# Optimization experiments

Measured on AMD Instinct MI355X. Metric: run time of the kernel, lower is better.

## Reference

```python
import jax, jax.numpy as jnp
import numpy as np

B, N, C = 2, 10000, 128
NH, NP = 4, 20          # n_heads, n_points (n_levels = 1)
DH = C // NH            # head dim = 32
HW = 100                # spatial shape (100, 100), N = HW*HW


def setup_inputs() -> dict:
    key = jax.random.key(0)
    ks = jax.random.split(key, 12)
    s = 0.05  # small param scale so softmax/linears stay well-conditioned
    return {
        "query": jax.random.normal(ks[0], (B, N, C), jnp.float32),
        "query_pos": jax.random.normal(ks[1], (B, N, C), jnp.float32),
        "W_val": jax.random.normal(ks[2], (C, C), jnp.float32) * s,
        "b_val": jax.random.normal(ks[3], (C,), jnp.float32) * s,
        "W_off": jax.random.normal(ks[4], (NH * NP * 2, C), jnp.float32) * s,
        "b_off": jax.random.normal(ks[5], (NH * NP * 2,), jnp.float32) * s,
        "W_attn": jax.random.normal(ks[6], (NH * NP, C), jnp.float32) * s,
        "b_attn": jax.random.normal(ks[7], (NH * NP,), jnp.float32) * s,
        "W_out1": jax.random.normal(ks[8], (C, C), jnp.float32) * s,
        "b_out1": jax.random.normal(ks[9], (C,), jnp.float32) * s,
        "W_out2": jax.random.normal(ks[10], (C, C), jnp.float32) * s,
        "b_out2": jax.random.normal(ks[11], (C,), jnp.float32) * s,
    }


def _msdeform_forward(query, query_pos, W_val, b_val, W_off, b_off,
                      W_attn, b_attn, W_out1, b_out1, W_out2, b_out2):
    residual = query
    q = query + query_pos  # pos added; value branch also uses q (query.clone())

    # reference points: meshgrid of (z, x) normalized to (0,1), shape (N, 2)
    lin = (jnp.arange(HW, dtype=jnp.float32) + 0.5) / HW
    ref_z, ref_x = jnp.meshgrid(lin, lin, indexing="ij")
    ref = jnp.stack([ref_z.reshape(-1), ref_x.reshape(-1)], axis=-1)  # (N,2)

    # projections
    value = (q @ W_val.T + b_val).reshape(B, N, NH, DH).transpose(0, 2, 1, 3)  # (B,NH,N,DH)
    off = (q @ W_off.T + b_off).reshape(B, N, NH, NP, 2)
    attn = jax.nn.softmax((q @ W_attn.T + b_attn).reshape(B, N, NH, NP), axis=-1)

    # sampling locations in normalized coords; offset normalizer = (W, H) = (100, 100)
    loc = ref[None, :, None, None, :] + off / HW  # (B,N,NH,NP,2)

    # grid_sample bilinear, align_corners=False, zeros padding:
    # pixel coord = loc * size - 0.5
    x = (loc[..., 0] * HW - 0.5).transpose(0, 2, 1, 3)  # (B,NH,N,NP)
    y = (loc[..., 1] * HW - 0.5).transpose(0, 2, 1, 3)
    aw = attn.transpose(0, 2, 1, 3)                     # (B,NH,N,NP)

    x0f = jnp.floor(x); y0f = jnp.floor(y)
    wx1 = x - x0f; wy1 = y - y0f
    wx0 = 1.0 - wx1; wy0 = 1.0 - wy1
    ix0 = x0f.astype(jnp.int32); iy0 = y0f.astype(jnp.int32)
    ix1 = ix0 + 1; iy1 = iy0 + 1

    def gather(ix, iy):
        valid = ((ix >= 0) & (ix < HW) & (iy >= 0) & (iy < HW)).astype(value.dtype)
        idx = jnp.clip(iy, 0, HW - 1) * HW + jnp.clip(ix, 0, HW - 1)  # (B,NH,N,NP)
        g = jnp.take_along_axis(value, idx.reshape(B, NH, N * NP, 1), axis=2)
        return g.reshape(B, NH, N, NP, DH) * valid[..., None]

    sampled = ((wx0 * wy0)[..., None] * gather(ix0, iy0)
               + (wx1 * wy0)[..., None] * gather(ix1, iy0)
               + (wx0 * wy1)[..., None] * gather(ix0, iy1)
               + (wx1 * wy1)[..., None] * gather(ix1, iy1))  # (B,NH,N,NP,DH)

    out = (sampled * aw[..., None]).sum(axis=3)             # (B,NH,N,DH)
    out = out.transpose(0, 2, 1, 3).reshape(B, N, C)
    out = out @ W_out1.T + b_out1   # MSDeformAttn.output_proj
    out = out @ W_out2.T + b_out2   # wrapper output_proj
    return out + residual           # dropout is identity in eval


def reference(query, query_pos, W_val, b_val, W_off, b_off,
              W_attn, b_attn, W_out1, b_out1, W_out2, b_out2):
    return _msdeform_forward(query, query_pos, W_val, b_val, W_off, b_off,
                             W_attn, b_attn, W_out1, b_out1, W_out2, b_out2)
```

## Files before the change

### kernel.cpp

```cpp
#include <hip/hip_runtime.h>
#include <hip/hip_bf16.h>
#include <math.h>

#define NTOK 10000
#define BATCH 2
#define CDIM 128
#define NHEAD 4
#define NPNT 20
#define DHEAD 32
#define HWDIM 100
#define MROWS (BATCH * NTOK)
#define OPAD 384
#define PHALO 4
#define TTILE 4
#define SPD 12
#define NPT 25
#define CELLPAD 40

typedef __attribute__((ext_vector_type(8))) short short8v;
typedef __attribute__((ext_vector_type(4))) short short4v;
typedef __attribute__((ext_vector_type(4))) float f32x4;

__device__ __forceinline__ float asf(unsigned u) {
  union { unsigned u; float f; } c; c.u = u; return c.f;
}

__device__ __forceinline__ void acc_cell(const __hip_bfloat16* p, float w,
                                         f32x4& a0, f32x4& a1) {
  int4 u = *(const int4*)p;
  f32x4 g0, g1;
  g0.x = asf(((unsigned)u.x) << 16); g0.y = asf(((unsigned)u.x) & 0xFFFF0000u);
  g0.z = asf(((unsigned)u.y) << 16); g0.w = asf(((unsigned)u.y) & 0xFFFF0000u);
  g1.x = asf(((unsigned)u.z) << 16); g1.y = asf(((unsigned)u.z) & 0xFFFF0000u);
  g1.z = asf(((unsigned)u.w) << 16); g1.w = asf(((unsigned)u.w) & 0xFFFF0000u);
  a0 += g0 * w;
  a1 += g1 * w;
}

__global__ __launch_bounds__(128) void prep_kernel(
    const float* __restrict__ W_val, const float* __restrict__ b_val,
    const float* __restrict__ W_off, const float* __restrict__ b_off,
    const float* __restrict__ W_attn, const float* __restrict__ b_attn,
    const float* __restrict__ W1, const float* __restrict__ b1,
    const float* __restrict__ W2, const float* __restrict__ b2,
    __hip_bfloat16* __restrict__ Wcat, float* __restrict__ bcat,
    __hip_bfloat16* __restrict__ Wc_bf, float* __restrict__ bc) {
  __shared__ float w2row[128];
  __shared__ float red[128];
  const int blk = blockIdx.x, c = threadIdx.x;
  if (blk < OPAD) {
    float v = 0.f, bv = 0.f;
    if (blk < 128) {
      v = W_val[blk * 128 + c]; bv = b_val[blk];
    } else {
      int h = (blk - 128) >> 6, k = (blk - 128) & 63;
      if (k < 40) { v = W_off[(h * 40 + k) * 128 + c]; bv = b_off[h * 40 + k]; }
      else if (k < 60) { v = W_attn[(h * 20 + k - 40) * 128 + c]; bv = b_attn[h * 20 + k - 40]; }
    }
    Wcat[(size_t)blk * 128 + c] = __float2bfloat16(v);
    if (c == 0) bcat[blk] = bv;
  } else {
    const int o = blk - OPAD;
    w2row[c] = W2[o * 128 + c];
    __syncthreads();
    float acc = 0.f;
    for (int k = 0; k < 128; ++k) acc += w2row[k] * W1[k * 128 + c];
    Wc_bf[(size_t)o * 128 + c] = __float2bfloat16(acc);
    red[c] = w2row[c] * b1[c];
    __syncthreads();
    for (int s = 64; s > 0; s >>= 1) {
      if (c < s) red[c] += red[c + s];
      __syncthreads();
    }
    if (c == 0) bc[o] = b2[o] + red[0];
  }
}

__global__ __launch_bounds__(256) void proj1_kernel(
    const float* __restrict__ query, const float* __restrict__ qpos,
    const __hip_bfloat16* __restrict__ Wcat, const float* __restrict__ bcat,
    __hip_bfloat16* __restrict__ value, __hip_bfloat16* __restrict__ offb,
    float* __restrict__ attnb) {
  __shared__ __hip_bfloat16 qa[64][128];
  __shared__ __hip_bfloat16 wb[64][128];
  const int t = threadIdx.x;
  const int r0 = blockIdx.x * 64;

#pragma unroll
  for (int i = 0; i < 4; ++i) {
    int lin = t + 256 * i;
    int r = lin >> 4, g = lin & 15;
    int c = g << 3;
    float4 v0 = make_float4(0.f, 0.f, 0.f, 0.f);
    float4 v1 = make_float4(0.f, 0.f, 0.f, 0.f);
    if (r0 + r < MROWS) {
      const float* p = query + (size_t)(r0 + r) * CDIM + c;
      v0 = *(const float4*)p;
      v1 = *(const float4*)(p + 4);
      const float* p2 = qpos + (size_t)(r0 + r) * CDIM + c;
      float4 u0 = *(const float4*)p2;
      float4 u1 = *(const float4*)(p2 + 4);
      v0.x += u0.x; v0.y += u0.y; v0.z += u0.z; v0.w += u0.w;
      v1.x += u1.x; v1.y += u1.y; v1.z += u1.z; v1.w += u1.w;
    }
    __hip_bfloat16* dst = &qa[r][(g ^ (r & 7)) << 3];
    dst[0] = __float2bfloat16(v0.x); dst[1] = __float2bfloat16(v0.y);
    dst[2] = __float2bfloat16(v0.z); dst[3] = __float2bfloat16(v0.w);
    dst[4] = __float2bfloat16(v1.x); dst[5] = __float2bfloat16(v1.y);
    dst[6] = __float2bfloat16(v1.z); dst[7] = __float2bfloat16(v1.w);
  }
  __syncthreads();

  const int wid = t >> 6;
  const int lane = t & 63;
  const int wr = (wid >> 1) * 32;
  const int wc = (wid & 1) * 32;
  const int lrow = lane & 15;
  const int lk = lane >> 4;

  short8v afr[4][2];
  {
    int ra0 = wr + lrow, ra1 = wr + 16 + lrow;
#pragma unroll
    for (int kk = 0; kk < 4; ++kk) {
      int gb = kk * 4 + lk;
      afr[kk][0] = *(const short8v*)&qa[ra0][(gb ^ (ra0 & 7)) << 3];
      afr[kk][1] = *(const short8v*)&qa[ra1][(gb ^ (ra1 & 7)) << 3];
    }
  }

  for (int ti = 0; ti < 3; ++ti) {
    const int ot = blockIdx.y * 192 + ti * 64;
    __syncthreads();
#pragma unroll
    for (int i = 0; i < 4; ++i) {
      int lin = t + 256 * i;
      int r = lin >> 4, g = lin & 15;
      short8v w = *(const short8v*)(Wcat + (size_t)(ot + r) * 128 + (g << 3));
      *(short8v*)&wb[r][(g ^ (r & 7)) << 3] = w;
    }
    __syncthreads();

    f32x4 acc[2][2];
#pragma unroll
    for (int mi = 0; mi < 2; ++mi)
#pragma unroll
      for (int ni = 0; ni < 2; ++ni) acc[mi][ni] = (f32x4)(0.f);

#pragma unroll
    for (int kk = 0; kk < 4; ++kk) {
      const int gb = kk * 4 + lk;
      int rb0 = wc + lrow, rb1 = wc + 16 + lrow;
      short8v b0 = *(const short8v*)&wb[rb0][(gb ^ (rb0 & 7)) << 3];
      short8v b1 = *(const short8v*)&wb[rb1][(gb ^ (rb1 & 7)) << 3];
      acc[0][0] = __builtin_amdgcn_mfma_f32_16x16x32_bf16(afr[kk][0], b0, acc[0][0], 0, 0, 0);
      acc[0][1] = __builtin_amdgcn_mfma_f32_16x16x32_bf16(afr[kk][0], b1, acc[0][1], 0, 0, 0);
      acc[1][0] = __builtin_amdgcn_mfma_f32_16x16x32_bf16(afr[kk][1], b0, acc[1][0], 0, 0, 0);
      acc[1][1] = __builtin_amdgcn_mfma_f32_16x16x32_bf16(afr[kk][1], b1, acc[1][1], 0, 0, 0);
    }

#pragma unroll
    for (int mi = 0; mi < 2; ++mi) {
#pragma unroll
      for (int ni = 0; ni < 2; ++ni) {
#pragma unroll
        for (int reg = 0; reg < 4; ++reg) {
          int r = r0 + wr + mi * 16 + (lane >> 4) * 4 + reg;
          int o = ot + wc + ni * 16 + (lane & 15);
          if (r >= MROWS) continue;
          float v = acc[mi][ni][reg] + bcat[o];
          int b = r >= NTOK ? 1 : 0;
          int n = r - b * NTOK;
          if (o < 128) {
            int h = o >> 5, rem = o & 31;
            value[(((size_t)b * NHEAD + h) * NTOK + n) * 32 + rem] =
                __float2bfloat16(v);
          } else {
            int h = (o - 128) >> 6, k = (o - 128) & 63;
            size_t base = ((size_t)(b * NHEAD + h) * NTOK + n);
            if (k < 40) {
              offb[base * 40 + k] = __float2bfloat16(v);
            } else if (k < 60) {
              attnb[base * 20 + (k - 40)] = v;
            }
          }
        }
      }
    }
  }
}

__global__ __launch_bounds__(256) void proj2_kernel(
    const __hip_bfloat16* __restrict__ outat,
    const __hip_bfloat16* __restrict__ Wc_bf, const float* __restrict__ bc,
    const float* __restrict__ resid, float* __restrict__ out) {
  __shared__ __hip_bfloat16 qa[64][128];
  __shared__ __hip_bfloat16 wb[64][128];
  const int t = threadIdx.x;
  const int r0 = blockIdx.x * 64;
  const int ot = blockIdx.y * 64;

#pragma unroll
  for (int i = 0; i < 4; ++i) {
    int lin = t + 256 * i;
    int r = lin >> 4, g = lin & 15;
    short8v v = (short8v)(short)0;
    if (r0 + r < MROWS)
      v = *(const short8v*)(outat + (size_t)(r0 + r) * CDIM + (g << 3));
    *(short8v*)&qa[r][(g ^ (r & 7)) << 3] = v;
  }
#pragma unroll
  for (int i = 0; i < 4; ++i) {
    int lin = t + 256 * i;
    int r = lin >> 4, g = lin & 15;
    short8v w = *(const short8v*)(Wc_bf + (size_t)(ot + r) * 128 + (g << 3));
    *(short8v*)&wb[r][(g ^ (r & 7)) << 3] = w;
  }
  __syncthreads();

  const int wid = t >> 6;
  const int lane = t & 63;
  const int wr = (wid >> 1) * 32;
  const int wc = (wid & 1) * 32;
  const int lrow = lane & 15;
  const int lk = lane >> 4;

  f32x4 acc[2][2];
#pragma unroll
  for (int mi = 0; mi < 2; ++mi)
#pragma unroll
    for (int ni = 0; ni < 2; ++ni) acc[mi][ni] = (f32x4)(0.f);

#pragma unroll
  for (int kk = 0; kk < 4; ++kk) {
    const int gb = kk * 4 + lk;
    int ra0 = wr + lrow, ra1 = wr + 16 + lrow;
    int rb0 = wc + lrow, rb1 = wc + 16 + lrow;
    short8v a0 = *(const short8v*)&qa[ra0][(gb ^ (ra0 & 7)) << 3];
    short8v a1 = *(const short8v*)&qa[ra1][(gb ^ (ra1 & 7)) << 3];
    short8v b0 = *(const short8v*)&wb[rb0][(gb ^ (rb0 & 7)) << 3];
    short8v b1 = *(const short8v*)&wb[rb1][(gb ^ (rb1 & 7)) << 3];
    acc[0][0] = __builtin_amdgcn_mfma_f32_16x16x32_bf16(a0, b0, acc[0][0], 0, 0, 0);
    acc[0][1] = __builtin_amdgcn_mfma_f32_16x16x32_bf16(a0, b1, acc[0][1], 0, 0, 0);
    acc[1][0] = __builtin_amdgcn_mfma_f32_16x16x32_bf16(a1, b0, acc[1][0], 0, 0, 0);
    acc[1][1] = __builtin_amdgcn_mfma_f32_16x16x32_bf16(a1, b1, acc[1][1], 0, 0, 0);
  }

#pragma unroll
  for (int mi = 0; mi < 2; ++mi) {
#pragma unroll
    for (int ni = 0; ni < 2; ++ni) {
#pragma unroll
      for (int reg = 0; reg < 4; ++reg) {
        int r = r0 + wr + mi * 16 + (lane >> 4) * 4 + reg;
        int o = ot + wc + ni * 16 + (lane & 15);
        if (r >= MROWS) continue;
        out[(size_t)r * CDIM + o] =
            acc[mi][ni][reg] + bc[o] + resid[(size_t)r * CDIM + o];
      }
    }
  }
}

__global__ __launch_bounds__(256) void sample_kernel(
    const __hip_bfloat16* __restrict__ value,
    const __hip_bfloat16* __restrict__ off, const float* __restrict__ attn,
    __hip_bfloat16* __restrict__ outat) {
  const int s = blockIdx.x & 7;
  const int pidx = blockIdx.x >> 3;
  const int PI = pidx % NPT, PJ = pidx / NPT;
  const int I0 = PI * TTILE, J0 = PJ * TTILE;
  const int b = s >> 2, h = s & 3;

  __shared__ __hip_bfloat16 patch[SPD * SPD][CELLPAD];
  const __hip_bfloat16* vglob = value + (size_t)s * NTOK * DHEAD;

  const int t = threadIdx.x;
  const int lane16 = t & 15;
  const int dg = lane16 & 3;
  const int pg = lane16 >> 2;
  const int tok = t >> 4;
  const int li = tok & 3, lj = tok >> 2;
  const int i = I0 + li, j = J0 + lj;
  const int n = i * HWDIM + j;

  unsigned ofu[5];
  float atf[5];
  {
    const unsigned* ob =
        (const unsigned*)(off + ((size_t)s * NTOK + n) * 40) + pg * 5;
    const float* ab = attn + ((size_t)s * NTOK + n) * 20 + pg * 5;
#pragma unroll
    for (int k = 0; k < 5; ++k) { ofu[k] = ob[k]; atf[k] = ab[k]; }
  }

#pragma unroll
  for (int it = 0; it < 3; ++it) {
    int lin = t + 256 * it;
    if (lin < SPD * SPD * 4) {
      int cell = lin >> 2, part = lin & 3;
      int py = cell / SPD, px = cell - py * SPD;
      int gy = J0 - PHALO + py;
      int gx = I0 - PHALO + px;
      short8v v = (short8v)(short)0;
      if (gy >= 0 && gy < HWDIM && gx >= 0 && gx < HWDIM)
        v = *(const short8v*)(vglob + ((size_t)(gy * HWDIM + gx)) * DHEAD +
                              part * 8);
      *(short8v*)&patch[cell][part * 8] = v;
    }
  }
  __syncthreads();

  float ssum = 0.f;
#pragma unroll
  for (int k = 0; k < 5; ++k) {
    atf[k] = __expf(atf[k]);
    ssum += atf[k];
  }

  const float fi = (float)i, fj = (float)j;
  f32x4 a0 = (f32x4)(0.f), a1 = (f32x4)(0.f);
  f32x4 e0 = (f32x4)(0.f), e1 = (f32x4)(0.f);
#pragma unroll
  for (int k = 0; k < 5; ++k) {
    const unsigned up = ofu[k];
    float x = fi + asf(up << 16);
    float y = fj + asf(up & 0xFFFF0000u);
    float aw = atf[k];
    float x0f = floorf(x), y0f = floorf(y);
    int ix0 = (int)x0f, iy0 = (int)y0f;
    float wx1 = x - x0f, wy1 = y - y0f;
    float wx0 = 1.f - wx1, wy0 = 1.f - wy1;
    float wya = aw * wy0, wyb = aw * wy1;
    float w00 = wya * wx0, w01 = wya * wx1;
    float w10 = wyb * wx0, w11 = wyb * wx1;
    int ly = iy0 - (J0 - PHALO);
    int lx = ix0 - (I0 - PHALO);
    if ((unsigned)ly <= SPD - 2 && (unsigned)lx <= SPD - 2) {
      const __hip_bfloat16* pb = &patch[ly * SPD + lx][dg * 8];
      acc_cell(pb, w00, a0, a1);
      acc_cell(pb + CELLPAD, w01, e0, e1);
      acc_cell(pb + SPD * CELLPAD, w10, a0, a1);
      acc_cell(pb + SPD * CELLPAD + CELLPAD, w11, e0, e1);
    } else {
      float wgt[4] = {w00, w01, w10, w11};
#pragma unroll
      for (int cy = 0; cy < 2; ++cy) {
        int iy = iy0 + cy;
        if (iy < 0 || iy >= HWDIM) continue;
#pragma unroll
        for (int cx = 0; cx < 2; ++cx) {
          int ix = ix0 + cx;
          if (ix < 0 || ix >= HWDIM) continue;
          acc_cell(vglob + ((size_t)(iy * HWDIM + ix)) * DHEAD + dg * 8,
                   wgt[cy * 2 + cx], a0, a1);
        }
      }
    }
  }
  f32x4 r0 = a0 + e0;
  f32x4 r1 = a1 + e1;

#pragma unroll
  for (int m = 4; m <= 8; m <<= 1) {
#pragma unroll
    for (int el = 0; el < 4; ++el) {
      r0[el] += __shfl_xor(r0[el], m);
      r1[el] += __shfl_xor(r1[el], m);
    }
    ssum += __shfl_xor(ssum, m);
  }

  if (pg == 0) {
    const float inv = 1.f / ssum;
    union { short8v v8; __hip_bfloat16 hh[8]; } o;
#pragma unroll
    for (int k = 0; k < 4; ++k) {
      o.hh[k] = __float2bfloat16(r0[k] * inv);
      o.hh[4 + k] = __float2bfloat16(r1[k] * inv);
    }
    *(short8v*)(outat + ((size_t)b * NTOK + n) * CDIM + h * DHEAD + dg * 8) =
        o.v8;
  }
}

extern "C" void kernel_launch(void* const* d_in, const int* in_sizes, int n_in,
                              void* d_out, int out_size, void* d_ws,
                              size_t ws_size, hipStream_t stream) {
  const float* query = (const float*)d_in[0];
  const float* query_pos = (const float*)d_in[1];
  const float* W_val = (const float*)d_in[2];
  const float* b_val = (const float*)d_in[3];
  const float* W_off = (const float*)d_in[4];
  const float* b_off = (const float*)d_in[5];
  const float* W_attn = (const float*)d_in[6];
  const float* b_attn = (const float*)d_in[7];
  const float* W_out1 = (const float*)d_in[8];
  const float* b_out1 = (const float*)d_in[9];
  const float* W_out2 = (const float*)d_in[10];
  const float* b_out2 = (const float*)d_in[11];
  float* out = (float*)d_out;

  char* ws = (char*)d_ws;
  __hip_bfloat16* value = (__hip_bfloat16*)ws;
  ws += (size_t)MROWS * CDIM * 2;
  __hip_bfloat16* offb = (__hip_bfloat16*)ws;
  ws += (size_t)MROWS * 160 * 2;
  float* attnb = (float*)ws;
  ws += (size_t)MROWS * 80 * 4;
  __hip_bfloat16* outat = (__hip_bfloat16*)ws;
  ws += (size_t)MROWS * CDIM * 2;
  float* bcat = (float*)ws; ws += OPAD * 4;
  float* bc = (float*)ws; ws += 128 * 4;
  __hip_bfloat16* Wcat = (__hip_bfloat16*)ws; ws += (size_t)OPAD * 128 * 2;
  __hip_bfloat16* Wc_bf = (__hip_bfloat16*)ws;

  prep_kernel<<<OPAD + 128, 128, 0, stream>>>(
      W_val, b_val, W_off, b_off, W_attn, b_attn, W_out1, b_out1, W_out2,
      b_out2, Wcat, bcat, Wc_bf, bc);

  proj1_kernel<<<dim3(313, 2), 256, 0, stream>>>(query, query_pos, Wcat, bcat,
                                                 value, offb, attnb);

  sample_kernel<<<8 * NPT * NPT, 256, 0, stream>>>(value, offb, attnb, outat);

  proj2_kernel<<<dim3(313, 2), 256, 0, stream>>>(outat, Wc_bf, bc, query, out);
}
```

Baseline: 58.95 us.

## Recast deformable sampling as dense weight-matrix times patch MFMA

The sampling kernel now scatters bilinear×attention weights into a per-token dense weight matrix over a 12x16 shared-memory patch using LDS atomics. It then multiplies that matrix by the transposed value patch with bf16 MFMA instructions. Tiles grow to 4x8 tokens, and out-of-patch samples fall back to per-element atomic accumulation from global memory. This trades the per-thread gather FMA work for matrix-core throughput, at the cost of LDS atomics, a transpose, extra barriers and bf16 rounding of the weights.

```diff
diff --git a/kernel.cpp b/kernel.cpp
--- a/kernel.cpp
+++ b/kernel.cpp
@@ -12,29 +12,20 @@
 #define MROWS (BATCH * NTOK)
 #define OPAD 384
 #define PHALO 4
-#define TTILE 4
-#define SPD 12
-#define NPT 25
-#define CELLPAD 40
+#define TI 4
+#define TJ 8
+#define SPI 12
+#define SPJ 16
+#define NPI 25
+#define NPJ 13
+#define NCELL 192
+#define WBS 200
 
 typedef __attribute__((ext_vector_type(8))) short short8v;
-typedef __attribute__((ext_vector_type(4))) short short4v;
 typedef __attribute__((ext_vector_type(4))) float f32x4;
 
 __device__ __forceinline__ float asf(unsigned u) {
   union { unsigned u; float f; } c; c.u = u; return c.f;
-}
-
-__device__ __forceinline__ void acc_cell(const __hip_bfloat16* p, float w,
-                                         f32x4& a0, f32x4& a1) {
-  int4 u = *(const int4*)p;
-  f32x4 g0, g1;
-  g0.x = asf(((unsigned)u.x) << 16); g0.y = asf(((unsigned)u.x) & 0xFFFF0000u);
-  g0.z = asf(((unsigned)u.y) << 16); g0.w = asf(((unsigned)u.y) & 0xFFFF0000u);
-  g1.x = asf(((unsigned)u.z) << 16); g1.y = asf(((unsigned)u.z) & 0xFFFF0000u);
-  g1.z = asf(((unsigned)u.w) << 16); g1.w = asf(((unsigned)u.w) & 0xFFFF0000u);
-  a0 += g0 * w;
-  a1 += g1 * w;
 }
 
 __global__ __launch_bounds__(128) void prep_kernel(
@@ -268,119 +259,176 @@
     __hip_bfloat16* __restrict__ outat) {
   const int s = blockIdx.x & 7;
   const int pidx = blockIdx.x >> 3;
-  const int PI = pidx % NPT, PJ = pidx / NPT;
-  const int I0 = PI * TTILE, J0 = PJ * TTILE;
+  const int PI = pidx % NPI, PJ = pidx / NPI;
+  const int I0 = PI * TI, J0 = PJ * TJ;
   const int b = s >> 2, h = s & 3;
 
-  __shared__ __hip_bfloat16 patch[SPD * SPD][CELLPAD];
+  __shared__ __align__(16) char smem[24576 + 12800 + 4096];
+  float* Wf = (float*)smem;
+  __hip_bfloat16* Wb = (__hip_bfloat16*)smem;
+  __hip_bfloat16* Vt = (__hip_bfloat16*)(smem + 24576);
+  float* fx = (float*)(smem + 24576 + 12800);
+
   const __hip_bfloat16* vglob = value + (size_t)s * NTOK * DHEAD;
-
   const int t = threadIdx.x;
-  const int lane16 = t & 15;
-  const int dg = lane16 & 3;
-  const int pg = lane16 >> 2;
-  const int tok = t >> 4;
+
+  int4 vl[3];
+#pragma unroll
+  for (int it = 0; it < 3; ++it) {
+    int task = t + 256 * it;
+    int cell = task >> 2, part = task & 3;
+    int py = cell / SPI, px = cell - py * SPI;
+    int gy = J0 - PHALO + py;
+    int gx = I0 - PHALO + px;
+    vl[it] = make_int4(0, 0, 0, 0);
+    if (gy >= 0 && gy < HWDIM && gx >= 0 && gx < HWDIM)
+      vl[it] = *(const int4*)(vglob + ((size_t)(gy * HWDIM + gx)) * DHEAD +
+                              part * 8);
+  }
+
+  const int tok = t >> 3, pg = t & 7;
   const int li = tok & 3, lj = tok >> 2;
   const int i = I0 + li, j = J0 + lj;
-  const int n = i * HWDIM + j;
-
-  unsigned ofu[5];
-  float atf[5];
+  const bool tv = (j < HWDIM);
+  const int n = tv ? (i * HWDIM + j) : 0;
+  unsigned ofu[3];
+  float atf[3];
+  int np = 0;
   {
-    const unsigned* ob =
-        (const unsigned*)(off + ((size_t)s * NTOK + n) * 40) + pg * 5;
-    const float* ab = attn + ((size_t)s * NTOK + n) * 20 + pg * 5;
-#pragma unroll
-    for (int k = 0; k < 5; ++k) { ofu[k] = ob[k]; atf[k] = ab[k]; }
-  }
+    const unsigned* ob = (const unsigned*)(off + ((size_t)s * NTOK + n) * 40);
+    const float* ab = attn + ((size_t)s * NTOK + n) * 20;
+#pragma unroll
+    for (int k = 0; k < 3; ++k) {
+      int p = pg + 8 * k;
+      if (p < NPNT) {
+        ofu[np] = ob[p];
+        atf[np] = ab[p];
+        ++np;
+      }
+    }
+  }
+
+  {
+    float4 z4 = make_float4(0.f, 0.f, 0.f, 0.f);
+    float4* wf4 = (float4*)Wf;
+#pragma unroll
+    for (int it = 0; it < 6; ++it) wf4[t + 256 * it] = z4;
+    ((float4*)fx)[t] = z4;
+  }
+
+  float ssum = 0.f;
+  for (int k = 0; k < np; ++k) { atf[k] = __expf(atf[k]); ssum += atf[k]; }
+  ssum += __shfl_xor(ssum, 1);
+  ssum += __shfl_xor(ssum, 2);
+  ssum += __shfl_xor(ssum, 4);
+  const float inv = tv ? (1.f / ssum) : 0.f;
+
+  __syncthreads();
 
 #pragma unroll
   for (int it = 0; it < 3; ++it) {
-    int lin = t + 256 * it;
-    if (lin < SPD * SPD * 4) {
-      int cell = lin >> 2, part = lin & 3;
-      int py = cell / SPD, px = cell - py * SPD;
-      int gy = J0 - PHALO + py;
-      int gx = I0 - PHALO + px;
-      short8v v = (short8v)(short)0;
-      if (gy >= 0 && gy < HWDIM && gx >= 0 && gx < HWDIM)
-        v = *(const short8v*)(vglob + ((size_t)(gy * HWDIM + gx)) * DHEAD +
-                              part * 8);
-      *(short8v*)&patch[cell][part * 8] = v;
-    }
-  }
-  __syncthreads();
-
-  float ssum = 0.f;
-#pragma unroll
-  for (int k = 0; k < 5; ++k) {
-    atf[k] = __expf(atf[k]);
-    ssum += atf[k];
+    int task = t + 256 * it;
+    int cell = task >> 2, part = task & 3;
+    union { int4 v4; __hip_bfloat16 hh[8]; } u;
+    u.v4 = vl[it];
+    int d0 = part * 8;
+#pragma unroll
+    for (int k = 0; k < 8; ++k) Vt[(d0 + k) * WBS + cell] = u.hh[k];
   }
 
   const float fi = (float)i, fj = (float)j;
-  f32x4 a0 = (f32x4)(0.f), a1 = (f32x4)(0.f);
-  f32x4 e0 = (f32x4)(0.f), e1 = (f32x4)(0.f);
-#pragma unroll
-  for (int k = 0; k < 5; ++k) {
-    const unsigned up = ofu[k];
-    float x = fi + asf(up << 16);
-    float y = fj + asf(up & 0xFFFF0000u);
-    float aw = atf[k];
-    float x0f = floorf(x), y0f = floorf(y);
-    int ix0 = (int)x0f, iy0 = (int)y0f;
-    float wx1 = x - x0f, wy1 = y - y0f;
-    float wx0 = 1.f - wx1, wy0 = 1.f - wy1;
-    float wya = aw * wy0, wyb = aw * wy1;
-    float w00 = wya * wx0, w01 = wya * wx1;
-    float w10 = wyb * wx0, w11 = wyb * wx1;
-    int ly = iy0 - (J0 - PHALO);
-    int lx = ix0 - (I0 - PHALO);
-    if ((unsigned)ly <= SPD - 2 && (unsigned)lx <= SPD - 2) {
-      const __hip_bfloat16* pb = &patch[ly * SPD + lx][dg * 8];
-      acc_cell(pb, w00, a0, a1);
-      acc_cell(pb + CELLPAD, w01, e0, e1);
-      acc_cell(pb + SPD * CELLPAD, w10, a0, a1);
-      acc_cell(pb + SPD * CELLPAD + CELLPAD, w11, e0, e1);
-    } else {
-      float wgt[4] = {w00, w01, w10, w11};
-#pragma unroll
-      for (int cy = 0; cy < 2; ++cy) {
-        int iy = iy0 + cy;
-        if (iy < 0 || iy >= HWDIM) continue;
-#pragma unroll
-        for (int cx = 0; cx < 2; ++cx) {
-          int ix = ix0 + cx;
-          if (ix < 0 || ix >= HWDIM) continue;
-          acc_cell(vglob + ((size_t)(iy * HWDIM + ix)) * DHEAD + dg * 8,
-                   wgt[cy * 2 + cx], a0, a1);
+  unsigned oob = 0;
+  if (tv) {
+    for (int k = 0; k < np; ++k) {
+      const unsigned up = ofu[k];
+      float x = fi + asf(up << 16);
+      float y = fj + asf(up & 0xFFFF0000u);
+      float aw = atf[k] * inv;
+      float x0f = floorf(x), y0f = floorf(y);
+      int ix0 = (int)x0f, iy0 = (int)y0f;
+      float wx1 = x - x0f, wy1 = y - y0f;
+      float wx0 = 1.f - wx1, wy0 = 1.f - wy1;
+      int ly = iy0 - (J0 - PHALO);
+      int lx = ix0 - (I0 - PHALO);
+      if ((unsigned)ly <= SPJ - 2 && (unsigned)lx <= SPI - 2) {
+        int cell = ly * SPI + lx;
+        float wya = aw * wy0, wyb = aw * wy1;
+        atomicAdd(&Wf[tok * NCELL + cell], wya * wx0);
+        atomicAdd(&Wf[tok * NCELL + cell + 1], wya * wx1);
+        atomicAdd(&Wf[tok * NCELL + cell + SPI], wyb * wx0);
+        atomicAdd(&Wf[tok * NCELL + cell + SPI + 1], wyb * wx1);
+      } else {
+        oob |= 1u << k;
+      }
+    }
+    if (oob) {
+      for (int k = 0; k < np; ++k) {
+        if (!(oob & (1u << k))) continue;
+        const unsigned up = ofu[k];
+        float x = fi + asf(up << 16);
+        float y = fj + asf(up & 0xFFFF0000u);
+        float aw = atf[k] * inv;
+        float x0f = floorf(x), y0f = floorf(y);
+        int ix0 = (int)x0f, iy0 = (int)y0f;
+        float wx1 = x - x0f, wy1 = y - y0f;
+        float wx0 = 1.f - wx1, wy0 = 1.f - wy1;
+        float wgt[4] = {aw * wy0 * wx0, aw * wy0 * wx1, aw * wy1 * wx0,
+                        aw * wy1 * wx1};
+        for (int cy = 0; cy < 2; ++cy) {
+          int iy = iy0 + cy;
+          if (iy < 0 || iy >= HWDIM) continue;
+          for (int cx = 0; cx < 2; ++cx) {
+            int ix = ix0 + cx;
+            if (ix < 0 || ix >= HWDIM) continue;
+            float w = wgt[cy * 2 + cx];
+            const __hip_bfloat16* vp =
+                vglob + ((size_t)(iy * HWDIM + ix)) * DHEAD;
+            for (int d = 0; d < 32; ++d)
+              atomicAdd(&fx[tok * 32 + d], w * __bfloat162float(vp[d]));
+          }
         }
       }
     }
   }
-  f32x4 r0 = a0 + e0;
-  f32x4 r1 = a1 + e1;
-
-#pragma unroll
-  for (int m = 4; m <= 8; m <<= 1) {
-#pragma unroll
-    for (int el = 0; el < 4; ++el) {
-      r0[el] += __shfl_xor(r0[el], m);
-      r1[el] += __shfl_xor(r1[el], m);
-    }
-    ssum += __shfl_xor(ssum, m);
-  }
-
-  if (pg == 0) {
-    const float inv = 1.f / ssum;
-    union { short8v v8; __hip_bfloat16 hh[8]; } o;
-#pragma unroll
-    for (int k = 0; k < 4; ++k) {
-      o.hh[k] = __float2bfloat16(r0[k] * inv);
-      o.hh[4 + k] = __float2bfloat16(r1[k] * inv);
-    }
-    *(short8v*)(outat + ((size_t)b * NTOK + n) * CDIM + h * DHEAD + dg * 8) =
-        o.v8;
+  __syncthreads();
+
+  {
+    int r = t & 31, chunk = t >> 5;
+    int c0 = chunk * 24;
+    float wreg[24];
+#pragma unroll
+    for (int cc = 0; cc < 24; ++cc) wreg[cc] = Wf[r * NCELL + c0 + cc];
+    __syncthreads();
+#pragma unroll
+    for (int cc = 0; cc < 24; ++cc)
+      Wb[r * WBS + c0 + cc] = __float2bfloat16(wreg[cc]);
+  }
+  __syncthreads();
+
+  const int wid = t >> 6;
+  const int lane = t & 63;
+  const int wr = (wid >> 1) * 16;
+  const int wc = (wid & 1) * 16;
+  const int arow = wr + (lane & 15);
+  const int bcol = wc + (lane & 15);
+  const int kbase = (lane >> 4) * 8;
+  f32x4 acc = (f32x4)(0.f);
+#pragma unroll
+  for (int ks = 0; ks < 6; ++ks) {
+    short8v a = *(const short8v*)&Wb[arow * WBS + ks * 32 + kbase];
+    short8v bfr = *(const short8v*)&Vt[bcol * WBS + ks * 32 + kbase];
+    acc = __builtin_amdgcn_mfma_f32_16x16x32_bf16(a, bfr, acc, 0, 0, 0);
+  }
+
+#pragma unroll
+  for (int reg = 0; reg < 4; ++reg) {
+    int tk = wr + (lane >> 4) * 4 + reg;
+    int d = bcol;
+    int jj = J0 + (tk >> 2);
+    if (jj >= HWDIM) continue;
+    int tn = (I0 + (tk & 3)) * HWDIM + jj;
+    float v = acc[reg] + fx[tk * 32 + d];
+    outat[((size_t)b * NTOK + tn) * CDIM + h * DHEAD + d] = __float2bfloat16(v);
   }
 }
 
@@ -422,7 +470,7 @@
   proj1_kernel<<<dim3(313, 2), 256, 0, stream>>>(query, query_pos, Wcat, bcat,
                                                  value, offb, attnb);
 
-  sample_kernel<<<8 * NPT * NPT, 256, 0, stream>>>(value, offb, attnb, outat);
+  sample_kernel<<<8 * NPI * NPJ, 256, 0, stream>>>(value, offb, attnb, outat);
 
   proj2_kernel<<<dim3(313, 2), 256, 0, stream>>>(outat, Wc_bf, bc, query, out);
 }
```

Result: slower. 94.85 us (+60.9%).
